# Optimization experiments

Hardware: AMD Instinct MI355X
Metric: run time of the kernel (lower is better)

Reference implementation:

```python
import jax, jax.numpy as jnp
import numpy as np

NUM_HEADS = 12
DIM = 768
HEAD_DIM = DIM // NUM_HEADS


def setup_inputs() -> dict:
    key = jax.random.key(0)
    ks = jax.random.split(key, 10)
    B, S = 4, 2048
    x = jax.random.normal(ks[0], (B, S, DIM), dtype=jnp.float32)
    attn_mask = jnp.zeros((B, S), dtype=jnp.float32)  # additive mask
    scale = 0.02
    Wq = jax.random.normal(ks[1], (DIM, DIM), dtype=jnp.float32) * scale
    bq = jnp.zeros((DIM,), dtype=jnp.float32)
    Wk = jax.random.normal(ks[2], (DIM, DIM), dtype=jnp.float32) * scale
    bk = jnp.zeros((DIM,), dtype=jnp.float32)
    Wv = jax.random.normal(ks[3], (DIM, DIM), dtype=jnp.float32) * scale
    bv = jnp.zeros((DIM,), dtype=jnp.float32)
    Wo = jax.random.normal(ks[4], (DIM, DIM), dtype=jnp.float32) * scale
    bo = jnp.zeros((DIM,), dtype=jnp.float32)
    return {"x": x, "attn_mask": attn_mask, "Wq": Wq, "bq": bq,
            "Wk": Wk, "bk": bk, "Wv": Wv, "bv": bv, "Wo": Wo, "bo": bo}


def reference(x, attn_mask, Wq, bq, Wk, bk, Wv, bv, Wo, bo):
    B, S, D = x.shape
    H, Hd = NUM_HEADS, HEAD_DIM
    scaling = Hd ** -0.5

    def split_heads(e):  # [B,S,D] -> [B,H,S,Hd]
        return e.reshape(B, S, H, Hd).transpose(0, 2, 1, 3)

    q = split_heads((x @ Wq + bq) * scaling)
    k = split_heads(x @ Wk + bk)
    v = split_heads(x @ Wv + bv)

    scores = jnp.einsum('bhqd,bhkd->bhqk', q, k)
    scores = scores + attn_mask[:, None, None, :]  # additive mask [B,1,1,S]
    probs = jax.nn.softmax(scores, axis=-1)
    out = jnp.einsum('bhqk,bhkd->bhqd', probs, v)  # [B,H,S,Hd]
    out = out.transpose(0, 2, 1, 3).reshape(B, S, D)
    return out @ Wo + bo
```

## Files before the change

kernel.cpp:

```cpp
#include <hip/hip_runtime.h>
#include <hip/hip_bf16.h>
#include <cstdint>
#include <cstddef>

#define DIM   768
#define NH    12
#define HD    64
#define BATCH 4
#define SEQ   2048
#define MTOT  (BATCH*SEQ)
#define NQKV  (3*DIM)

#define LOG2E 1.4426950408889634f

typedef __attribute__((ext_vector_type(8))) short bf16x8;
typedef __attribute__((ext_vector_type(4))) short bf16x4;
typedef __attribute__((ext_vector_type(4))) float f32x4;

__device__ __forceinline__ short f2bf(float f){
  union { __hip_bfloat16 h; short s; } u;
  u.h = __float2bfloat16(f);
  return u.s;
}

#if defined(__HIP_DEVICE_COMPILE__) && __has_builtin(__builtin_amdgcn_exp2f)
#define EXP2(x) __builtin_amdgcn_exp2f(x)
#else
#define EXP2(x) exp2f(x)
#endif

__device__ __forceinline__ f32x4 mfma32(bf16x8 a, bf16x8 b, f32x4 c){
  return __builtin_amdgcn_mfma_f32_16x16x32_bf16(a, b, c, 0, 0, 0);
}

__device__ __forceinline__ void gl_lds16(const short* g, short* l){
  __builtin_amdgcn_global_load_lds(
      (const __attribute__((address_space(1))) unsigned int*)g,
      (__attribute__((address_space(3))) unsigned int*)l,
      16, 0, 0);
}

#define VMCNT(N) asm volatile("s_waitcnt vmcnt(" #N ")" ::: "memory")
#define BARRIER() __builtin_amdgcn_s_barrier()

__device__ __forceinline__ size_t img_idx(int m, int k){
  const int mt = m >> 7, r = m & 127, ks = k >> 5, c = k & 31;
  return ((size_t)(mt*24 + ks))*4096 + (size_t)((r>>6)*2048 + ((r>>4)&3)*512
       + ((r&15) + ((c>>3)<<4))*8 + (c&7));
}


__global__ __launch_bounds__(256) void pack_all(
    const float* __restrict__ x,
    const float* __restrict__ Wq, const float* __restrict__ Wk,
    const float* __restrict__ Wv, const float* __restrict__ Wo,
    const float* __restrict__ bq, const float* __restrict__ bk,
    const float* __restrict__ bv, const float* __restrict__ mask,
    short* __restrict__ xb, short* __restrict__ wqkv, short* __restrict__ wot,
    float* __restrict__ bqkv, float* __restrict__ mask2)
{
  const int NX4 = MTOT*DIM/4;
  const int NW4 = DIM*DIM/4;
  int gid = blockIdx.x * 256 + threadIdx.x;

  if (gid < NX4){
    float4 v = ((const float4*)x)[gid];
    const int e = gid*4;
    const int m = e / DIM, k = e - m*DIM;
    bf16x4 o;
    o[0] = f2bf(v.x); o[1] = f2bf(v.y); o[2] = f2bf(v.z); o[3] = f2bf(v.w);
    *(bf16x4*)&xb[img_idx(m, k)] = o;
    return;
  }
  gid -= NX4;
  if (gid < 4*NW4){
    const int mat = gid / NW4;
    const int rem = gid - mat*NW4;
    const int e = rem*4;
    const int k = e / DIM, n = e - k*DIM;
    const float* W = (mat == 0) ? Wq : (mat == 1) ? Wk : (mat == 2) ? Wv : Wo;
    const float4 v = *(const float4*)&W[e];
    short* img = (mat < 3) ? wqkv : wot;
    const int ng = (mat < 3) ? mat*DIM + n : n;
    img[img_idx(ng+0, k)] = f2bf(v.x);
    img[img_idx(ng+1, k)] = f2bf(v.y);
    img[img_idx(ng+2, k)] = f2bf(v.z);
    img[img_idx(ng+3, k)] = f2bf(v.w);
    return;
  }
  gid -= 4*NW4;
  if (gid < NQKV)
    bqkv[gid] = (gid < DIM) ? bq[gid] : (gid < 2*DIM) ? bk[gid-DIM] : bv[gid-2*DIM];
  if (gid < BATCH*SEQ)
    mask2[gid] = mask[gid] * LOG2E;
}


template<int MODE>
__global__ __launch_bounds__(256, 3) void gemm_lds(
    const short* __restrict__ Aimg,
    const short* __restrict__ Bimg,
    const float* __restrict__ bias,
    short* __restrict__ o0, short* __restrict__ o1, short* __restrict__ o2,
    float* __restrict__ fo)
{
  __shared__ short ldsA[3*4096];
  __shared__ short ldsB[3*4096];

  const int tid = threadIdx.x;
  const int w  = tid >> 6, l = tid & 63;
  const int lr = l & 15,  lg = l >> 4;
  const int wr = w >> 1,  wc = w & 1;
  const int mt = blockIdx.x, nt = blockIdx.y;
  const int mBase = mt * 128;
  const int nBase = nt * 128;

  const short* gA = Aimg + (size_t)mt*24*4096 + w*512 + l*8;
  const short* gB = Bimg + (size_t)nt*24*4096 + w*512 + l*8;

#define STAGE(BUF, KS) do {                                                \
    gl_lds16(gA + (KS)*4096,        &ldsA[(BUF)*4096 + w*512]);            \
    gl_lds16(gA + (KS)*4096 + 2048, &ldsA[(BUF)*4096 + 2048 + w*512]);     \
    gl_lds16(gB + (KS)*4096,        &ldsB[(BUF)*4096 + w*512]);            \
    gl_lds16(gB + (KS)*4096 + 2048, &ldsB[(BUF)*4096 + 2048 + w*512]);     \
  } while(0)

#define GCOMP(CUR) do {                                                    \
    bf16x8 a[4], b[4];                                                     \
    _Pragma("unroll")                                                      \
    for (int i = 0; i < 4; ++i){                                           \
      a[i] = *(const bf16x8*)&ldsA[(CUR)*4096 + wr*2048 + i*512 + l*8];    \
      b[i] = *(const bf16x8*)&ldsB[(CUR)*4096 + wc*2048 + i*512 + l*8];    \
    }                                                                      \
    _Pragma("unroll")                                                      \
    for (int i = 0; i < 4; ++i)                                            \
      _Pragma("unroll")                                                    \
      for (int j = 0; j < 4; ++j)                                          \
        acc[i][j] = mfma32(a[i], b[j], acc[i][j]);                         \
  } while(0)

  f32x4 acc[4][4] = {};
  STAGE(0, 0);
  STAGE(1, 1);
  int cur = 0;
  for (int kt = 0; kt < 23; ++kt){
    VMCNT(4);
    BARRIER();
    if (kt < 22){
      int nb = cur + 2; if (nb >= 3) nb -= 3;
      STAGE(nb, kt+2);
    }
    GCOMP(cur);
    cur = (cur == 2) ? 0 : cur + 1;
  }
  VMCNT(0);
  BARRIER();
  GCOMP(cur);
#undef STAGE
#undef GCOMP

  if (MODE == 0){
    const int sect  = nBase / DIM;
    const int nloc0 = nBase - sect*DIM + wc*64;
    const float scl = (sect == 0) ? 0.125f*LOG2E : 1.0f;
#pragma unroll
    for (int j = 0; j < 4; ++j){
      const int nl = nloc0 + j*16 + lr;
      const int h = nl >> 6, d = nl & (HD-1);
      const float bn = bias[nBase + wc*64 + j*16 + lr];
#pragma unroll
      for (int i = 0; i < 4; ++i){
        const int m0 = mBase + wr*64 + i*16 + lg*4;
        const int b_ = m0 >> 11, s0 = m0 & (SEQ-1);
        const int bh = b_*NH + h;
        if (sect == 2){
          const int p0 = (((s0>>2)&3)<<3) | (((s0>>4)&1)<<2);
          const size_t idx = (((size_t)bh*64 + (s0>>5))*4 + (d>>4))*512
                           + ((d&15) + (p0>>3)*16)*8 + (p0&7);
          bf16x4 ov;
#pragma unroll
          for (int r = 0; r < 4; ++r) ov[r] = f2bf((acc[i][j][r] + bn));
          *(bf16x4*)&o2[idx] = ov;
        } else {
#pragma unroll
          for (int r = 0; r < 4; ++r){
            const int s_ = s0 + r;
            const float val = (acc[i][j][r] + bn) * scl;
            if (sect == 0){
              o0[((size_t)bh*SEQ + s_)*HD + d] = f2bf(val);
            } else {
              const size_t idx = (((size_t)bh*64 + (s_>>5))*4
                                  + ((s_>>4)&1)*2 + (d>>5))*512
                               + ((s_&15) + ((d>>3)&3)*16)*8 + (d&7);
              o1[idx] = f2bf(val);
            }
          }
        }
      }
    }
  } else {
#pragma unroll
    for (int j = 0; j < 4; ++j){
      const int n = nBase + wc*64 + j*16 + lr;
      const float bn = bias[n];
#pragma unroll
      for (int i = 0; i < 4; ++i){
#pragma unroll
        for (int r = 0; r < 4; ++r){
          const int m = mBase + wr*64 + i*16 + lg*4 + r;
          fo[(size_t)m * DIM + n] = acc[i][j][r] + bn;
        }
      }
    }
  }
}


__global__ __launch_bounds__(256, 3) void attn_kernel(
    const short* __restrict__ q,
    const short* __restrict__ kimg,
    const short* __restrict__ vimg,
    const float* __restrict__ mask2,
    short* __restrict__ ao)
{
  __shared__ short ldsK[3*4096];
  __shared__ short ldsV[3*4096];

  const int tid = threadIdx.x;
  const int l = tid & 63, w = tid >> 6;
  const int lr = l & 15, lg = l >> 4;
  const int bh = blockIdx.x;
  const int b_ = bh / NH;
  const int h  = bh - b_*NH;
  const int qbase = blockIdx.y * 128 + w * 32;

  const short* qh   = q + (size_t)bh * SEQ * HD;
  const short* kSrc = kimg + (size_t)bh * 64 * 2048 + w*512 + l*8;
  const short* vSrc = vimg + (size_t)bh * 64 * 2048 + w*512 + l*8;
  const float* mRow = mask2 + (size_t)b_ * SEQ + lg*4;

  bf16x8 qf[2][2];
#pragma unroll
  for (int t = 0; t < 2; ++t){
    qf[t][0] = *(const bf16x8*)&qh[(size_t)(qbase + t*16 + lr)*HD + lg*8];
    qf[t][1] = *(const bf16x8*)&qh[(size_t)(qbase + t*16 + lr)*HD + 32 + lg*8];
  }

  bf16x8 ones;
#pragma unroll
  for (int j = 0; j < 8; ++j) ones[j] = (short)0x3F80;

  f32x4 o[2][4] = {};
  f32x4 lacc[2] = {};

#define ASTAGE(BUF, ST) do {                                                 \
    gl_lds16(kSrc + (size_t)(ST)*4096,        &ldsK[(BUF)*4096 + w*512]);    \
    gl_lds16(kSrc + (size_t)(ST)*4096 + 2048, &ldsK[(BUF)*4096+2048+w*512]); \
    gl_lds16(vSrc + (size_t)(ST)*4096,        &ldsV[(BUF)*4096 + w*512]);    \
    gl_lds16(vSrc + (size_t)(ST)*4096 + 2048, &ldsV[(BUF)*4096+2048+w*512]); \
  } while(0)

#define ACOMP(MA, MB, MC, MD, CUR) do {                                     \
    _Pragma("unroll")                                                        \
    for (int sub = 0; sub < 2; ++sub){                                       \
      bf16x8 kf[4], vf[4];                                                   \
      _Pragma("unroll")                                                      \
      for (int f = 0; f < 4; ++f){                                           \
        kf[f] = *(const bf16x8*)&ldsK[(CUR)*4096 + sub*2048 + f*512 + l*8];  \
        vf[f] = *(const bf16x8*)&ldsV[(CUR)*4096 + sub*2048 + f*512 + l*8];  \
      }                                                                      \
      const float4 m0 = sub ? (MC) : (MA);                                   \
      const float4 m1 = sub ? (MD) : (MB);                                   \
      bf16x8 pf[2];                                                          \
      _Pragma("unroll")                                                      \
      for (int t = 0; t < 2; ++t){                                           \
        f32x4 s0 = {m0.x, m0.y, m0.z, m0.w};                                 \
        f32x4 s1 = {m1.x, m1.y, m1.z, m1.w};                                 \
        s0 = mfma32(kf[0], qf[t][0], s0);                                    \
        s0 = mfma32(kf[1], qf[t][1], s0);                                    \
        s1 = mfma32(kf[2], qf[t][0], s1);                                    \
        s1 = mfma32(kf[3], qf[t][1], s1);                                    \
        const float p0 = EXP2(s0[0]);                                        \
        const float p1 = EXP2(s0[1]);                                        \
        const float p2 = EXP2(s0[2]);                                        \
        const float p3 = EXP2(s0[3]);                                        \
        const float p4 = EXP2(s1[0]);                                        \
        const float p5 = EXP2(s1[1]);                                        \
        const float p6 = EXP2(s1[2]);                                        \
        const float p7 = EXP2(s1[3]);                                        \
        pf[t][0]=f2bf(p0); pf[t][1]=f2bf(p1); pf[t][2]=f2bf(p2); pf[t][3]=f2bf(p3); \
        pf[t][4]=f2bf(p4); pf[t][5]=f2bf(p5); pf[t][6]=f2bf(p6); pf[t][7]=f2bf(p7); \
      }                                                                      \
      __builtin_amdgcn_s_setprio(1);                                         \
      _Pragma("unroll")                                                      \
      for (int dblk = 0; dblk < 4; ++dblk){                                  \
        o[0][dblk] = mfma32(vf[dblk], pf[0], o[0][dblk]);                    \
        o[1][dblk] = mfma32(vf[dblk], pf[1], o[1][dblk]);                    \
      }                                                                      \
      lacc[0] = mfma32(ones, pf[0], lacc[0]);                                \
      lacc[1] = mfma32(ones, pf[1], lacc[1]);                                \
      __builtin_amdgcn_s_setprio(0);                                         \
    }                                                                        \
  } while(0)

  ASTAGE(0, 0);
  ASTAGE(1, 1);
  int cur = 0;
  for (int st = 0; st < 31; ++st){
    VMCNT(4);
    BARRIER();
    const float4 mva = *(const float4*)(mRow + st*64);
    const float4 mvb = *(const float4*)(mRow + st*64 + 16);
    const float4 mvc = *(const float4*)(mRow + st*64 + 32);
    const float4 mvd = *(const float4*)(mRow + st*64 + 48);
    asm volatile("" ::: "memory");
    if (st < 30){
      int nb = cur + 2; if (nb >= 3) nb -= 3;
      ASTAGE(nb, st+2);
    }
    ACOMP(mva, mvb, mvc, mvd, cur);
    cur = (cur == 2) ? 0 : cur + 1;
  }
  VMCNT(0);
  BARRIER();
  {
    const float4 mva = *(const float4*)(mRow + 31*64);
    const float4 mvb = *(const float4*)(mRow + 31*64 + 16);
    const float4 mvc = *(const float4*)(mRow + 31*64 + 32);
    const float4 mvd = *(const float4*)(mRow + 31*64 + 48);
    ACOMP(mva, mvb, mvc, mvd, cur);
  }
#undef ASTAGE
#undef ACOMP

#pragma unroll
  for (int t = 0; t < 2; ++t){
    const float rinv = 1.f / lacc[t][0];
    const int m = b_*SEQ + qbase + t*16 + lr;
    const int mt = m >> 7, r = m & 127;
    short* abase = ao + (size_t)mt*24*4096
                 + (r>>6)*2048 + ((r>>4)&3)*512;
#pragma unroll
    for (int dblk = 0; dblk < 4; ++dblk){
      bf16x4 ov;
#pragma unroll
      for (int rr = 0; rr < 4; ++rr) ov[rr] = f2bf(o[t][dblk][rr] * rinv);
      const int k = h*64 + dblk*16 + lg*4;
      const int ks = k >> 5, c = k & 31;
      *(bf16x4*)&abase[(size_t)ks*4096 + ((r&15) + ((c>>3)<<4))*8 + (c&7)] = ov;
    }
  }
}


extern "C" void kernel_launch(void* const* d_in, const int* in_sizes, int n_in,
                              void* d_out, int out_size, void* d_ws, size_t ws_size,
                              hipStream_t stream) {
  const float* x    = (const float*)d_in[0];
  const float* mask = (const float*)d_in[1];
  const float* Wq   = (const float*)d_in[2];
  const float* bq   = (const float*)d_in[3];
  const float* Wk   = (const float*)d_in[4];
  const float* bk   = (const float*)d_in[5];
  const float* Wv   = (const float*)d_in[6];
  const float* bv   = (const float*)d_in[7];
  const float* Wo   = (const float*)d_in[8];
  const float* bo   = (const float*)d_in[9];
  float* out = (float*)d_out;

  char* ws = (char*)d_ws;
  const size_t SZ_XB = (size_t)MTOT * DIM * sizeof(short);
  const size_t SZ_W  = (size_t)DIM * DIM * sizeof(short);

  short* xb   = (short*)ws;            ws += SZ_XB;
  short* wqkv = (short*)ws;            ws += 3*SZ_W;
  short* wot  = (short*)ws;            ws += SZ_W;
  short* qb   = (short*)ws;            ws += SZ_XB;
  short* kimg = (short*)ws;            ws += SZ_XB;
  short* vimg = (short*)ws;            ws += SZ_XB;
  short* ao   = (short*)ws;            ws += SZ_XB;
  float* bqkv = (float*)ws;            ws += NQKV * sizeof(float);
  float* mask2= (float*)ws;            ws += (size_t)BATCH*SEQ*sizeof(float);

  const int NPACK = MTOT*DIM/4 + DIM*DIM + BATCH*SEQ;
  pack_all<<<(NPACK + 255)/256, 256, 0, stream>>>(
      x, Wq, Wk, Wv, Wo, bq, bk, bv, mask, xb, wqkv, wot, bqkv, mask2);

  dim3 qkvgrid(MTOT/128, NQKV/128);
  gemm_lds<0><<<qkvgrid, 256, 0, stream>>>(xb, wqkv, bqkv, qb, kimg, vimg, nullptr);

  dim3 agrid(BATCH*NH, SEQ/128);
  attn_kernel<<<agrid, 256, 0, stream>>>(qb, kimg, vimg, mask2, ao);

  dim3 ogrid(MTOT/128, DIM/128);
  gemm_lds<1><<<ogrid, 256, 0, stream>>>(ao, wot, bo, nullptr, nullptr, nullptr, out);
}
```

Measured before the change: 146.5 us.

## Enlarge GEMM block tile to 256x128 with 512 threads sharing B tile

Both projection GEMMs now use 512-thread blocks covering 256 rows by 128 columns, so each staged B (weight) tile is reused by twice as many rows. The global-to-LDS staging is redistributed so each of the 8 waves issues 3 loads per k-step, and the wait count is adjusted to match. This cuts weight-tile traffic and halves the block count, at the cost of more LDS per block, lower occupancy (2 blocks per CU) and fewer blocks, which may hurt tail balance on the smaller output GEMM.

```diff
diff --git a/kernel.cpp b/kernel.cpp
--- a/kernel.cpp
+++ b/kernel.cpp
@@ -97,46 +97,56 @@
 
 
 template<int MODE>
-__global__ __launch_bounds__(256, 3) void gemm_lds(
+__global__ __launch_bounds__(512, 2) void gemm_lds(
     const short* __restrict__ Aimg,
     const short* __restrict__ Bimg,
     const float* __restrict__ bias,
     short* __restrict__ o0, short* __restrict__ o1, short* __restrict__ o2,
     float* __restrict__ fo)
 {
-  __shared__ short ldsA[3*4096];
+  __shared__ short ldsA[3*8192];
   __shared__ short ldsB[3*4096];
 
   const int tid = threadIdx.x;
   const int w  = tid >> 6, l = tid & 63;
   const int lr = l & 15,  lg = l >> 4;
   const int wr = w >> 1,  wc = w & 1;
-  const int mt = blockIdx.x, nt = blockIdx.y;
-  const int mBase = mt * 128;
-  const int nBase = nt * 128;
-
-  const short* gA = Aimg + (size_t)mt*24*4096 + w*512 + l*8;
-  const short* gB = Bimg + (size_t)nt*24*4096 + w*512 + l*8;
-
-#define STAGE(BUF, KS) do {                                                \
-    gl_lds16(gA + (KS)*4096,        &ldsA[(BUF)*4096 + w*512]);            \
-    gl_lds16(gA + (KS)*4096 + 2048, &ldsA[(BUF)*4096 + 2048 + w*512]);     \
-    gl_lds16(gB + (KS)*4096,        &ldsB[(BUF)*4096 + w*512]);            \
-    gl_lds16(gB + (KS)*4096 + 2048, &ldsB[(BUF)*4096 + 2048 + w*512]);     \
+  const int bt = blockIdx.x, nt = blockIdx.y;
+  const int mBase = bt * 256 + wr * 64;
+  const int nB    = nt * 128;
+
+  const short* gA0 = Aimg + (size_t)(2*bt  )*24*4096;
+  const short* gA1 = Aimg + (size_t)(2*bt+1)*24*4096;
+  const short* gB  = Bimg + (size_t)nt*24*4096;
+
+#define STAGE(BUF, KS) do {                                                  \
+    _Pragma("unroll")                                                        \
+    for (int j_ = 0; j_ < 3; ++j_){                                          \
+      const int c_ = w*3 + j_;                                               \
+      if (c_ < 8)                                                            \
+        gl_lds16(gA0 + (size_t)(KS)*4096 + c_*512 + l*8,                     \
+                 &ldsA[(BUF)*8192 + c_*512]);                                \
+      else if (c_ < 16)                                                      \
+        gl_lds16(gA1 + (size_t)(KS)*4096 + (c_-8)*512 + l*8,                 \
+                 &ldsA[(BUF)*8192 + c_*512]);                                \
+      else                                                                   \
+        gl_lds16(gB  + (size_t)(KS)*4096 + (c_-16)*512 + l*8,                \
+                 &ldsB[(BUF)*4096 + (c_-16)*512]);                           \
+    }                                                                        \
   } while(0)
 
-#define GCOMP(CUR) do {                                                    \
-    bf16x8 a[4], b[4];                                                     \
-    _Pragma("unroll")                                                      \
-    for (int i = 0; i < 4; ++i){                                           \
-      a[i] = *(const bf16x8*)&ldsA[(CUR)*4096 + wr*2048 + i*512 + l*8];    \
-      b[i] = *(const bf16x8*)&ldsB[(CUR)*4096 + wc*2048 + i*512 + l*8];    \
-    }                                                                      \
-    _Pragma("unroll")                                                      \
-    for (int i = 0; i < 4; ++i)                                            \
-      _Pragma("unroll")                                                    \
-      for (int j = 0; j < 4; ++j)                                          \
-        acc[i][j] = mfma32(a[i], b[j], acc[i][j]);                         \
+#define GCOMP(CUR) do {                                                      \
+    bf16x8 a[4], b[4];                                                       \
+    _Pragma("unroll")                                                        \
+    for (int i = 0; i < 4; ++i){                                             \
+      a[i] = *(const bf16x8*)&ldsA[(CUR)*8192 + wr*2048 + i*512 + l*8];      \
+      b[i] = *(const bf16x8*)&ldsB[(CUR)*4096 + wc*2048 + i*512 + l*8];      \
+    }                                                                        \
+    _Pragma("unroll")                                                        \
+    for (int i = 0; i < 4; ++i)                                              \
+      _Pragma("unroll")                                                      \
+      for (int j = 0; j < 4; ++j)                                            \
+        acc[i][j] = mfma32(a[i], b[j], acc[i][j]);                           \
   } while(0)
 
   f32x4 acc[4][4] = {};
@@ -144,7 +154,7 @@
   STAGE(1, 1);
   int cur = 0;
   for (int kt = 0; kt < 23; ++kt){
-    VMCNT(4);
+    VMCNT(3);
     BARRIER();
     if (kt < 22){
       int nb = cur + 2; if (nb >= 3) nb -= 3;
@@ -160,17 +170,17 @@
 #undef GCOMP
 
   if (MODE == 0){
-    const int sect  = nBase / DIM;
-    const int nloc0 = nBase - sect*DIM + wc*64;
+    const int sect  = nB / DIM;
+    const int nloc0 = nB - sect*DIM + wc*64;
     const float scl = (sect == 0) ? 0.125f*LOG2E : 1.0f;
 #pragma unroll
     for (int j = 0; j < 4; ++j){
       const int nl = nloc0 + j*16 + lr;
       const int h = nl >> 6, d = nl & (HD-1);
-      const float bn = bias[nBase + wc*64 + j*16 + lr];
+      const float bn = bias[nB + wc*64 + j*16 + lr];
 #pragma unroll
       for (int i = 0; i < 4; ++i){
-        const int m0 = mBase + wr*64 + i*16 + lg*4;
+        const int m0 = mBase + i*16 + lg*4;
         const int b_ = m0 >> 11, s0 = m0 & (SEQ-1);
         const int bh = b_*NH + h;
         if (sect == 2){
@@ -201,13 +211,13 @@
   } else {
 #pragma unroll
     for (int j = 0; j < 4; ++j){
-      const int n = nBase + wc*64 + j*16 + lr;
+      const int n = nB + wc*64 + j*16 + lr;
       const float bn = bias[n];
 #pragma unroll
       for (int i = 0; i < 4; ++i){
 #pragma unroll
         for (int r = 0; r < 4; ++r){
-          const int m = mBase + wr*64 + i*16 + lg*4 + r;
+          const int m = mBase + i*16 + lg*4 + r;
           fo[(size_t)m * DIM + n] = acc[i][j][r] + bn;
         }
       }
@@ -386,12 +396,12 @@
   pack_all<<<(NPACK + 255)/256, 256, 0, stream>>>(
       x, Wq, Wk, Wv, Wo, bq, bk, bv, mask, xb, wqkv, wot, bqkv, mask2);
 
-  dim3 qkvgrid(MTOT/128, NQKV/128);
-  gemm_lds<0><<<qkvgrid, 256, 0, stream>>>(xb, wqkv, bqkv, qb, kimg, vimg, nullptr);
+  dim3 qkvgrid(MTOT/256, NQKV/128);
+  gemm_lds<0><<<qkvgrid, 512, 0, stream>>>(xb, wqkv, bqkv, qb, kimg, vimg, nullptr);
 
   dim3 agrid(BATCH*NH, SEQ/128);
   attn_kernel<<<agrid, 256, 0, stream>>>(qb, kimg, vimg, mask2, ao);
 
-  dim3 ogrid(MTOT/128, DIM/128);
-  gemm_lds<1><<<ogrid, 256, 0, stream>>>(ao, wot, bo, nullptr, nullptr, nullptr, out);
-}
+  dim3 ogrid(MTOT/256, DIM/128);
+  gemm_lds<1><<<ogrid, 512, 0, stream>>>(ao, wot, bo, nullptr, nullptr, nullptr, out);
+}
```

Result: slower. 168.2 us (+14.9%).
